# Performance work log

Hardware: AMD Instinct MI355X
Metric: run time of the kernel (lower is better)

The kernel has to match this reference:

```python
import jax, jax.numpy as jnp
import numpy as np

B, H, W, C = 4, 64, 64, 512
CR = C // 8  # reduced channel dim for query/key (conv_b, conv_c)


def setup_inputs() -> dict:
    key = jax.random.key(0)
    k1, k2, k3, k4, k5 = jax.random.split(key, 5)
    x = jax.random.normal(k1, (B, H, W, C), dtype=jnp.float32)
    # 1x1 conv kernels (no bias) == dense weights applied per pixel
    Wb = jax.random.normal(k2, (C, CR), dtype=jnp.float32) * (2.0 / C) ** 0.5
    Wc = jax.random.normal(k3, (C, CR), dtype=jnp.float32) * (2.0 / C) ** 0.5
    Wd = jax.random.normal(k4, (C, C), dtype=jnp.float32) * (2.0 / C) ** 0.5
    gamma = jax.random.normal(k5, (1,), dtype=jnp.float32)
    return {"x": x, "Wb": Wb, "Wc": Wc, "Wd": Wd, "gamma": gamma}


def reference(x, Wb, Wc, Wd, gamma):
    b, h, w, c = x.shape
    n = h * w
    xf = x.reshape(b, n, c)                       # [B,N,C] flatten spatial
    q = jnp.einsum('bnc,cd->bnd', xf, Wb)         # conv_b: [B,N,CR]
    k = jnp.einsum('bnc,cd->bnd', xf, Wc)         # conv_c: [B,N,CR]
    v = jnp.einsum('bnc,cd->bnd', xf, Wd)         # conv_d: [B,N,C]
    scores = jnp.einsum('bnd,bmd->bnm', q, k)     # [B,N,N] position affinities
    attn = jax.nn.softmax(scores, axis=-1)
    out = jnp.einsum('bnm,bmc->bnc', attn, v)     # [B,N,C]
    out = out.reshape(b, h, w, c)
    return gamma * out + x
```

## Files before the change

kernel.cpp:

```cpp
#include <hip/hip_runtime.h>


typedef __bf16 bf16_t;
typedef __bf16 bf16x8 __attribute__((ext_vector_type(8)));
typedef float f32x4 __attribute__((ext_vector_type(4)));
typedef unsigned long long u64;

#define NN 4096
#define CC 512
#define VSTRIDE 4160u
#define PSTRIDE 4160u
#define ESHIFT 90.0f

#define OFF_QH 0u
#define OFF_QL 1048576u
#define OFF_KH 2097152u
#define OFF_KL 3145728u
#define OFF_VT 4194304u
#define OFF_WBH 29491200u
#define OFF_WBL 29523968u
#define OFF_WCH 29556736u
#define OFF_WCL 29589504u
#define OFF_WD  29622272u
#define OFF_P   12713984u
#define PBATCH  17039360u

static __device__ __forceinline__ f32x4 mfma16(bf16x8 a, bf16x8 b, f32x4 c) {
    return __builtin_amdgcn_mfma_f32_16x16x32_bf16(a, b, c, 0, 0, 0);
}

static __device__ __forceinline__ void load_lds16(const bf16_t* g, bf16_t* l) {
    __builtin_amdgcn_global_load_lds(
        (const __attribute__((address_space(1))) unsigned int*)g,
        (__attribute__((address_space(3))) unsigned int*)l, 16, 0, 0);
}

__global__ __launch_bounds__(256) void prep_kernel(const float* __restrict__ Wb,
                                                   const float* __restrict__ Wc,
                                                   const float* __restrict__ Wd,
                                                   bf16_t* __restrict__ ws) {
    int j = blockIdx.x * 256 + threadIdx.x;
    if (j < 32768) {
        int n = j >> 9, k = j & 511;
        float v = Wb[k * 64 + n];
        bf16_t h = (bf16_t)v;
        ws[OFF_WBH + j] = h;
        ws[OFF_WBL + j] = (bf16_t)(v - (float)h);
    } else if (j < 65536) {
        int j2 = j - 32768;
        int n = j2 >> 9, k = j2 & 511;
        float v = Wc[k * 64 + n];
        bf16_t h = (bf16_t)v;
        ws[OFF_WCH + j2] = h;
        ws[OFF_WCL + j2] = (bf16_t)(v - (float)h);
    } else if (j < 327680) {
        int j2 = j - 65536;
        int n = j2 >> 9, k = j2 & 511;
        ws[OFF_WD + j2] = (bf16_t)Wd[k * 512 + n];
    }
}

__global__ __launch_bounds__(256, 1) void qkv_kernel(const float* __restrict__ x,
                                                     bf16_t* __restrict__ ws) {
    int mt = blockIdx.x;
    int g  = blockIdx.y;
    int tid = threadIdx.x;
    int w = tid >> 6, lane = tid & 63, quad = lane >> 4, l16 = lane & 15;

    __shared__ __align__(16) bf16_t Vs[64][72];

    const float* xrow = x + (size_t)(mt * 64 + w * 16 + l16) * 512 + quad * 8;

    if (g < 2) {
        bf16x8 xh[16], xl[16];
#pragma unroll
        for (int ks = 0; ks < 16; ++ks) {
            f32x4 a0 = *(const f32x4*)(xrow + ks * 32);
            f32x4 a1 = *(const f32x4*)(xrow + ks * 32 + 4);
#pragma unroll
            for (int j = 0; j < 4; ++j) {
                bf16_t h0 = (bf16_t)a0[j];
                bf16_t h1 = (bf16_t)a1[j];
                xh[ks][j] = h0;     xl[ks][j] = (bf16_t)(a0[j] - (float)h0);
                xh[ks][4 + j] = h1; xl[ks][4 + j] = (bf16_t)(a1[j] - (float)h1);
            }
        }

        const bf16_t* wh = ws + (g == 0 ? OFF_WBH : OFF_WCH);
        const bf16_t* wl = ws + (g == 0 ? OFF_WBL : OFF_WCL);
        f32x4 acc[4];
#pragma unroll
        for (int nt = 0; nt < 4; ++nt) acc[nt] = (f32x4){0.f, 0.f, 0.f, 0.f};
#pragma unroll
        for (int ks = 0; ks < 16; ++ks) {
#pragma unroll
            for (int nt = 0; nt < 4; ++nt) {
                size_t wo = (size_t)(nt * 16 + l16) * 512 + ks * 32 + quad * 8;
                bf16x8 bh = *(const bf16x8*)(wh + wo);
                bf16x8 bl = *(const bf16x8*)(wl + wo);
                acc[nt] = mfma16(xh[ks], bh, acc[nt]);
                acc[nt] = mfma16(xh[ks], bl, acc[nt]);
                acc[nt] = mfma16(xl[ks], bh, acc[nt]);
            }
        }
        unsigned base_h = (g == 0) ? OFF_QH : OFF_KH;
        unsigned base_l = (g == 0) ? OFF_QL : OFF_KL;
#pragma unroll
        for (int nt = 0; nt < 4; ++nt) {
            int gc = nt * 16 + l16;
#pragma unroll
            for (int r = 0; r < 4; ++r) {
                int gr = mt * 64 + w * 16 + quad * 4 + r;
                int b = gr >> 12, np = gr & 4095;
                float v = acc[nt][r];
                bf16_t h = (bf16_t)v;
                size_t o = ((size_t)(b * 4096 + np)) * 64 + gc;
                ws[base_h + o] = h;
                ws[base_l + o] = (bf16_t)(v - (float)h);
            }
        }
    } else {
        bf16x8 xh[16];
#pragma unroll
        for (int ks = 0; ks < 16; ++ks) {
            f32x4 a0 = *(const f32x4*)(xrow + ks * 32);
            f32x4 a1 = *(const f32x4*)(xrow + ks * 32 + 4);
#pragma unroll
            for (int j = 0; j < 4; ++j) {
                xh[ks][j] = (bf16_t)a0[j];
                xh[ks][4 + j] = (bf16_t)a1[j];
            }
        }

        for (int t = 0; t < 2; ++t) {
            int nT = (g - 2) * 2 + t;
            const bf16_t* wp = ws + OFF_WD + (size_t)nT * 64 * 512;
            f32x4 acc[4];
#pragma unroll
            for (int nt = 0; nt < 4; ++nt) acc[nt] = (f32x4){0.f, 0.f, 0.f, 0.f};
#pragma unroll
            for (int ks = 0; ks < 16; ++ks) {
#pragma unroll
                for (int nt = 0; nt < 4; ++nt) {
                    bf16x8 bb = *(const bf16x8*)(wp + (size_t)(nt * 16 + l16) * 512 + ks * 32 + quad * 8);
                    acc[nt] = mfma16(xh[ks], bb, acc[nt]);
                }
            }
#pragma unroll
            for (int nt = 0; nt < 4; ++nt) {
                bf16_t pk[4];
#pragma unroll
                for (int r = 0; r < 4; ++r) pk[r] = (bf16_t)acc[nt][r];
                *(u64*)&Vs[nt * 16 + l16][w * 16 + quad * 4] = *(u64*)pk;
            }
            __syncthreads();
            int gr0 = mt * 64;
            int bb = gr0 >> 12, np0 = gr0 & 4095;
            int ch = tid >> 2, seg = tid & 3;
            f32x4 d0 = *(const f32x4*)&Vs[ch][seg * 16];
            f32x4 d1 = *(const f32x4*)&Vs[ch][seg * 16 + 8];
            bf16_t* dst = ws + OFF_VT +
                ((size_t)bb * 512 + (size_t)(nT * 64 + ch)) * VSTRIDE + np0 + seg * 16;
            *(f32x4*)(dst) = d0;
            *(f32x4*)(dst + 8) = d1;
            __syncthreads();
        }
    }
}

__global__ __launch_bounds__(256, 2) void score_kernel(bf16_t* __restrict__ ws) {
    int idx = blockIdx.x;
    int mt = idx & 31;
    int nt = (idx >> 5) & 31;
    int b  = idx >> 10;
    int tid = threadIdx.x;
    int w = tid >> 6, lane = tid & 63, quad = lane >> 4, l16 = lane & 15;
    int wr = w >> 1, wc = w & 1;

    __shared__ __align__(16) bf16_t Ls[128][136];

    const bf16_t* Qh = ws + OFF_QH + (size_t)b * NN * 64;
    const bf16_t* Ql = ws + OFF_QL + (size_t)b * NN * 64;
    const bf16_t* Kh = ws + OFF_KH + (size_t)b * NN * 64;
    const bf16_t* Kl = ws + OFF_KL + (size_t)b * NN * 64;

    bf16x8 qh[4][2], ql[4][2];
#pragma unroll
    for (int rt = 0; rt < 4; ++rt) {
        size_t qo = (size_t)(nt * 128 + wr * 64 + rt * 16 + l16) * 64 + quad * 8;
        qh[rt][0] = *(const bf16x8*)(Qh + qo);
        qh[rt][1] = *(const bf16x8*)(Qh + qo + 32);
        ql[rt][0] = *(const bf16x8*)(Ql + qo);
        ql[rt][1] = *(const bf16x8*)(Ql + qo + 32);
    }

    f32x4 s[4][4];
#pragma unroll
    for (int ct = 0; ct < 4; ++ct) {
        size_t ko = (size_t)(mt * 128 + wc * 64 + ct * 16 + l16) * 64 + quad * 8;
        bf16x8 kh0 = *(const bf16x8*)(Kh + ko);
        bf16x8 kh1 = *(const bf16x8*)(Kh + ko + 32);
        bf16x8 kl0 = *(const bf16x8*)(Kl + ko);
        bf16x8 kl1 = *(const bf16x8*)(Kl + ko + 32);
#pragma unroll
        for (int rt = 0; rt < 4; ++rt) {
            f32x4 a = (f32x4){0.f, 0.f, 0.f, 0.f};
            a = mfma16(qh[rt][0], kh0, a);
            a = mfma16(qh[rt][1], kh1, a);
            a = mfma16(qh[rt][0], kl0, a);
            a = mfma16(qh[rt][1], kl1, a);
            a = mfma16(ql[rt][0], kh0, a);
            a = mfma16(ql[rt][1], kh1, a);
            s[rt][ct] = a;
        }
    }

#pragma unroll
    for (int rt = 0; rt < 4; ++rt)
#pragma unroll
        for (int ct = 0; ct < 4; ++ct)
#pragma unroll
            for (int r = 0; r < 4; ++r) {
                float p = __expf(s[rt][ct][r] - ESHIFT);
                Ls[wr * 64 + rt * 16 + quad * 4 + r][wc * 64 + ct * 16 + l16] = (bf16_t)p;
            }
    __syncthreads();

    bf16_t* P = ws + OFF_P + (size_t)b * PBATCH;
    int row0 = tid >> 4, chunk = tid & 15;
#pragma unroll
    for (int it = 0; it < 8; ++it) {
        int row = it * 16 + row0;
        f32x4 d = *(const f32x4*)&Ls[row][chunk * 8];
        *(f32x4*)(P + (size_t)(nt * 128 + row) * PSTRIDE + mt * 128 + chunk * 8) = d;
    }
}

__global__ __launch_bounds__(256, 2) void pv_kernel(const float* __restrict__ x,
                                                    const float* __restrict__ gamma_p,
                                                    const bf16_t* __restrict__ ws,
                                                    float* __restrict__ out) {
    int idx = blockIdx.x;
    int ct4 = idx & 3;
    int b   = (idx >> 2) & 3;
    int nt  = idx >> 4;
    int tid = threadIdx.x;
    int w = tid >> 6, lane = tid & 63, quad = lane >> 4, l16 = lane & 15;
    int wr = w >> 1, wc = w & 1;

    __shared__ __align__(16) bf16_t Pt[2][8192];
    __shared__ __align__(16) bf16_t Vt[2][8192];

    const bf16_t* P = ws + OFF_P + (size_t)b * PBATCH + (size_t)(nt * 128) * PSTRIDE;
    const bf16_t* V = ws + OFF_VT + (size_t)b * CC * VSTRIDE + (size_t)(ct4 * 128) * VSTRIDE;

    int sr = tid >> 3;
    int sc = (tid & 7) ^ (sr & 7);
    const bf16_t* gp = P + (size_t)sr * PSTRIDE + sc * 8;
    const bf16_t* gv = V + (size_t)sr * VSTRIDE + sc * 8;

    f32x4 o[4][4];
#pragma unroll
    for (int rt = 0; rt < 4; ++rt)
#pragma unroll
        for (int ct = 0; ct < 4; ++ct) o[rt][ct] = (f32x4){0.f, 0.f, 0.f, 0.f};
    f32x4 osum[4];
#pragma unroll
    for (int rt = 0; rt < 4; ++rt) osum[rt] = (f32x4){0.f, 0.f, 0.f, 0.f};

    bf16_t onev = (bf16_t)1.0f;
    bf16x8 vones = {onev, onev, onev, onev, onev, onev, onev, onev};

    auto stage = [&](int buf, int t) {
        int m0 = t * 64;
        load_lds16(gp + m0,                  &Pt[buf][tid * 8]);
        load_lds16(gp + 32u * PSTRIDE + m0,  &Pt[buf][2048 + tid * 8]);
        load_lds16(gp + 64u * PSTRIDE + m0,  &Pt[buf][4096 + tid * 8]);
        load_lds16(gp + 96u * PSTRIDE + m0,  &Pt[buf][6144 + tid * 8]);
        load_lds16(gv + m0,                  &Vt[buf][tid * 8]);
        load_lds16(gv + 32u * VSTRIDE + m0,  &Vt[buf][2048 + tid * 8]);
        load_lds16(gv + 64u * VSTRIDE + m0,  &Vt[buf][4096 + tid * 8]);
        load_lds16(gv + 96u * VSTRIDE + m0,  &Vt[buf][6144 + tid * 8]);
    };

    auto compute = [&](int buf) {
#pragma unroll
        for (int kk = 0; kk < 2; ++kk) {
            bf16x8 pa[4], vb[4];
#pragma unroll
            for (int rt = 0; rt < 4; ++rt) {
                int R = wr * 64 + rt * 16 + l16;
                int mc = (kk * 4 + quad) ^ (R & 7);
                pa[rt] = *(const bf16x8*)&Pt[buf][R * 64 + mc * 8];
            }
#pragma unroll
            for (int ct = 0; ct < 4; ++ct) {
                int Rv = wc * 64 + ct * 16 + l16;
                int mc = (kk * 4 + quad) ^ (Rv & 7);
                vb[ct] = *(const bf16x8*)&Vt[buf][Rv * 64 + mc * 8];
            }
#pragma unroll
            for (int ct = 0; ct < 4; ++ct)
#pragma unroll
                for (int rt = 0; rt < 4; ++rt)
                    o[rt][ct] = mfma16(pa[rt], vb[ct], o[rt][ct]);
            if (wc == 0) {
#pragma unroll
                for (int rt = 0; rt < 4; ++rt)
                    osum[rt] = mfma16(pa[rt], vones, osum[rt]);
            }
        }
    };

    stage(0, 0);
    __syncthreads();
    for (int t = 0; t < 63; ++t) {
        int cur = t & 1;
        stage(cur ^ 1, t + 1);
        compute(cur);
        __syncthreads();
    }
    compute(1);

    float* rsum_s = (float*)&Pt[0][0];
    if (wc == 0 && l16 == 0) {
#pragma unroll
        for (int rt = 0; rt < 4; ++rt)
#pragma unroll
            for (int r = 0; r < 4; ++r)
                rsum_s[wr * 64 + rt * 16 + quad * 4 + r] = osum[rt][r];
    }
    __syncthreads();

    float g = gamma_p[0];
#pragma unroll
    for (int rt = 0; rt < 4; ++rt) {
        f32x4 rs = *(const f32x4*)&rsum_s[wr * 64 + rt * 16 + quad * 4];
        f32x4 linv;
#pragma unroll
        for (int r = 0; r < 4; ++r) linv[r] = 1.0f / rs[r];
#pragma unroll
        for (int ct = 0; ct < 4; ++ct) {
#pragma unroll
            for (int r = 0; r < 4; ++r) {
                int n = nt * 128 + wr * 64 + rt * 16 + quad * 4 + r;
                int c = ct4 * 128 + wc * 64 + ct * 16 + l16;
                size_t off = ((size_t)(b * 4096 + n)) * 512 + c;
                out[off] = g * (o[rt][ct][r] * linv[r]) + x[off];
            }
        }
    }
}

extern "C" void kernel_launch(void* const* d_in, const int* in_sizes, int n_in,
                              void* d_out, int out_size, void* d_ws, size_t ws_size,
                              hipStream_t stream) {
    const float* x     = (const float*)d_in[0];
    const float* Wb    = (const float*)d_in[1];
    const float* Wc    = (const float*)d_in[2];
    const float* Wd    = (const float*)d_in[3];
    const float* gamma = (const float*)d_in[4];
    bf16_t* ws = (bf16_t*)d_ws;
    float* out = (float*)d_out;

    prep_kernel<<<1280, 256, 0, stream>>>(Wb, Wc, Wd, ws);
    qkv_kernel<<<dim3(256, 6), 256, 0, stream>>>(x, ws);
    score_kernel<<<4096, 256, 0, stream>>>(ws);
    pv_kernel<<<512, 256, 0, stream>>>(x, gamma, ws, out);
}
```

Baseline: 359.9 us.

## Pre-split x into bf16 hi/lo fragment layout and prepack weights for MFMA

Adds an xprep kernel that converts x once into bf16 hi/lo halves stored in MFMA-fragment order, and changes weight prep to write fragment-ordered bf16x8 packs. qkv_kernel then reads contiguous per-lane 16-byte fragments instead of strided fp32 rows, so the six y-groups no longer each repeat the conversion. The cost is an extra launch plus writing and re-reading about 16 MB of converted x through the workspace.

```diff
diff --git a/kernel.cpp b/kernel.cpp
--- a/kernel.cpp
+++ b/kernel.cpp
@@ -22,6 +22,8 @@
 #define OFF_WCH 29556736u
 #define OFF_WCL 29589504u
 #define OFF_WD  29622272u
+#define OFF_XHF 46137344u
+#define OFF_XLF 54525952u
 #define OFF_P   12713984u
 #define PBATCH  17039360u
 
@@ -40,28 +42,64 @@
                                                    const float* __restrict__ Wd,
                                                    bf16_t* __restrict__ ws) {
     int j = blockIdx.x * 256 + threadIdx.x;
-    if (j < 32768) {
-        int n = j >> 9, k = j & 511;
-        float v = Wb[k * 64 + n];
-        bf16_t h = (bf16_t)v;
-        ws[OFF_WBH + j] = h;
-        ws[OFF_WBL + j] = (bf16_t)(v - (float)h);
-    } else if (j < 65536) {
-        int j2 = j - 32768;
-        int n = j2 >> 9, k = j2 & 511;
-        float v = Wc[k * 64 + n];
-        bf16_t h = (bf16_t)v;
-        ws[OFF_WCH + j2] = h;
-        ws[OFF_WCL + j2] = (bf16_t)(v - (float)h);
-    } else if (j < 327680) {
-        int j2 = j - 65536;
-        int n = j2 >> 9, k = j2 & 511;
-        ws[OFF_WD + j2] = (bf16_t)Wd[k * 512 + n];
-    }
-}
-
-__global__ __launch_bounds__(256, 1) void qkv_kernel(const float* __restrict__ x,
-                                                     bf16_t* __restrict__ ws) {
+    if (j < 8192) {
+        const float* W = (j < 4096) ? Wb : Wc;
+        unsigned oh = (j < 4096) ? OFF_WBH : OFF_WCH;
+        unsigned ol = (j < 4096) ? OFF_WBL : OFF_WCL;
+        int jc = j & 4095;
+        int nt = jc >> 10, ks = (jc >> 6) & 15, lane = jc & 63;
+        int quad = lane >> 4, l16 = lane & 15;
+        int col = nt * 16 + l16, k0 = ks * 32 + quad * 8;
+        bf16x8 h, l;
+#pragma unroll
+        for (int i = 0; i < 8; ++i) {
+            float v = W[(k0 + i) * 64 + col];
+            bf16_t hv = (bf16_t)v;
+            h[i] = hv;
+            l[i] = (bf16_t)(v - (float)hv);
+        }
+        *(bf16x8*)(ws + oh + (size_t)jc * 8) = h;
+        *(bf16x8*)(ws + ol + (size_t)jc * 8) = l;
+    } else if (j < 40960) {
+        int jc = j - 8192;
+        int nT = jc >> 12, nt = (jc >> 10) & 3, ks = (jc >> 6) & 15, lane = jc & 63;
+        int quad = lane >> 4, l16 = lane & 15;
+        int col = nT * 64 + nt * 16 + l16, k0 = ks * 32 + quad * 8;
+        bf16x8 h;
+#pragma unroll
+        for (int i = 0; i < 8; ++i)
+            h[i] = (bf16_t)Wd[(k0 + i) * 512 + col];
+        *(bf16x8*)(ws + OFF_WD + (size_t)jc * 8) = h;
+    }
+}
+
+__global__ __launch_bounds__(256) void xprep_kernel(const float* __restrict__ x,
+                                                    bf16_t* __restrict__ ws) {
+    int mt = blockIdx.x;
+    int tid = threadIdx.x;
+    const float* xb = x + (size_t)mt * 32768;
+#pragma unroll
+    for (int it = 0; it < 16; ++it) {
+        int c = it * 256 + tid;
+        int row = c >> 6, col8 = c & 63;
+        f32x4 a0 = *(const f32x4*)(xb + c * 8);
+        f32x4 a1 = *(const f32x4*)(xb + c * 8 + 4);
+        bf16x8 h, l;
+#pragma unroll
+        for (int jj = 0; jj < 4; ++jj) {
+            bf16_t h0 = (bf16_t)a0[jj];
+            bf16_t h1 = (bf16_t)a1[jj];
+            h[jj] = h0;     l[jj] = (bf16_t)(a0[jj] - (float)h0);
+            h[4 + jj] = h1; l[4 + jj] = (bf16_t)(a1[jj] - (float)h1);
+        }
+        int w = row >> 4, l16 = row & 15, ks = col8 >> 2, quad = col8 & 3;
+        size_t dst = (size_t)mt * 32768 + w * 8192 + ks * 512 + (quad * 16 + l16) * 8;
+        *(bf16x8*)(ws + OFF_XHF + dst) = h;
+        *(bf16x8*)(ws + OFF_XLF + dst) = l;
+    }
+}
+
+__global__ __launch_bounds__(256, 1) void qkv_kernel(bf16_t* __restrict__ ws) {
     int mt = blockIdx.x;
     int g  = blockIdx.y;
     int tid = threadIdx.x;
@@ -69,35 +107,28 @@
 
     __shared__ __align__(16) bf16_t Vs[64][72];
 
-    const float* xrow = x + (size_t)(mt * 64 + w * 16 + l16) * 512 + quad * 8;
+    size_t xoff = (size_t)mt * 32768 + w * 8192 + lane * 8;
 
     if (g < 2) {
         bf16x8 xh[16], xl[16];
 #pragma unroll
+        for (int ks = 0; ks < 16; ++ks)
+            xh[ks] = *(const bf16x8*)(ws + OFF_XHF + xoff + ks * 512);
+#pragma unroll
+        for (int ks = 0; ks < 16; ++ks)
+            xl[ks] = *(const bf16x8*)(ws + OFF_XLF + xoff + ks * 512);
+
+        const bf16_t* whf = ws + (g == 0 ? OFF_WBH : OFF_WCH) + lane * 8;
+        const bf16_t* wlf = ws + (g == 0 ? OFF_WBL : OFF_WCL) + lane * 8;
+        f32x4 acc[4];
+#pragma unroll
+        for (int nt = 0; nt < 4; ++nt) acc[nt] = (f32x4){0.f, 0.f, 0.f, 0.f};
+#pragma unroll
         for (int ks = 0; ks < 16; ++ks) {
-            f32x4 a0 = *(const f32x4*)(xrow + ks * 32);
-            f32x4 a1 = *(const f32x4*)(xrow + ks * 32 + 4);
-#pragma unroll
-            for (int j = 0; j < 4; ++j) {
-                bf16_t h0 = (bf16_t)a0[j];
-                bf16_t h1 = (bf16_t)a1[j];
-                xh[ks][j] = h0;     xl[ks][j] = (bf16_t)(a0[j] - (float)h0);
-                xh[ks][4 + j] = h1; xl[ks][4 + j] = (bf16_t)(a1[j] - (float)h1);
-            }
-        }
-
-        const bf16_t* wh = ws + (g == 0 ? OFF_WBH : OFF_WCH);
-        const bf16_t* wl = ws + (g == 0 ? OFF_WBL : OFF_WCL);
-        f32x4 acc[4];
-#pragma unroll
-        for (int nt = 0; nt < 4; ++nt) acc[nt] = (f32x4){0.f, 0.f, 0.f, 0.f};
-#pragma unroll
-        for (int ks = 0; ks < 16; ++ks) {
 #pragma unroll
             for (int nt = 0; nt < 4; ++nt) {
-                size_t wo = (size_t)(nt * 16 + l16) * 512 + ks * 32 + quad * 8;
-                bf16x8 bh = *(const bf16x8*)(wh + wo);
-                bf16x8 bl = *(const bf16x8*)(wl + wo);
+                bf16x8 bh = *(const bf16x8*)(whf + (nt * 16 + ks) * 512);
+                bf16x8 bl = *(const bf16x8*)(wlf + (nt * 16 + ks) * 512);
                 acc[nt] = mfma16(xh[ks], bh, acc[nt]);
                 acc[nt] = mfma16(xh[ks], bl, acc[nt]);
                 acc[nt] = mfma16(xl[ks], bh, acc[nt]);
@@ -122,19 +153,12 @@
     } else {
         bf16x8 xh[16];
 #pragma unroll
-        for (int ks = 0; ks < 16; ++ks) {
-            f32x4 a0 = *(const f32x4*)(xrow + ks * 32);
-            f32x4 a1 = *(const f32x4*)(xrow + ks * 32 + 4);
-#pragma unroll
-            for (int j = 0; j < 4; ++j) {
-                xh[ks][j] = (bf16_t)a0[j];
-                xh[ks][4 + j] = (bf16_t)a1[j];
-            }
-        }
+        for (int ks = 0; ks < 16; ++ks)
+            xh[ks] = *(const bf16x8*)(ws + OFF_XHF + xoff + ks * 512);
 
         for (int t = 0; t < 2; ++t) {
             int nT = (g - 2) * 2 + t;
-            const bf16_t* wp = ws + OFF_WD + (size_t)nT * 64 * 512;
+            const bf16_t* wdf = ws + OFF_WD + lane * 8;
             f32x4 acc[4];
 #pragma unroll
             for (int nt = 0; nt < 4; ++nt) acc[nt] = (f32x4){0.f, 0.f, 0.f, 0.f};
@@ -142,7 +166,7 @@
             for (int ks = 0; ks < 16; ++ks) {
 #pragma unroll
                 for (int nt = 0; nt < 4; ++nt) {
-                    bf16x8 bb = *(const bf16x8*)(wp + (size_t)(nt * 16 + l16) * 512 + ks * 32 + quad * 8);
+                    bf16x8 bb = *(const bf16x8*)(wdf + (size_t)(((nT * 4 + nt) * 16 + ks)) * 512);
                     acc[nt] = mfma16(xh[ks], bb, acc[nt]);
                 }
             }
@@ -363,8 +387,9 @@
     bf16_t* ws = (bf16_t*)d_ws;
     float* out = (float*)d_out;
 
-    prep_kernel<<<1280, 256, 0, stream>>>(Wb, Wc, Wd, ws);
-    qkv_kernel<<<dim3(256, 6), 256, 0, stream>>>(x, ws);
+    prep_kernel<<<160, 256, 0, stream>>>(Wb, Wc, Wd, ws);
+    xprep_kernel<<<256, 256, 0, stream>>>(x, ws);
+    qkv_kernel<<<dim3(256, 6), 256, 0, stream>>>(ws);
     score_kernel<<<4096, 256, 0, stream>>>(ws);
     pv_kernel<<<512, 256, 0, stream>>>(x, gamma, ws, out);
 }
```

Measured after the change: 307.2 us. -14.6%, faster.
